# Kernel optimization log

Hardware: AMD Instinct MI355X
Metric: run time of the kernel (lower is better)

Reference implementation:

```python
import jax, jax.numpy as jnp
import numpy as np

N = 4096
INPUT_SIZE = 1024
HIDDEN = 512


def setup_inputs() -> dict:
    key = jax.random.key(0)
    ks = jax.random.split(key, 7)
    s_in = 1.0 / np.sqrt(INPUT_SIZE)
    return {
        "embs": jax.random.normal(ks[0], (N, INPUT_SIZE), dtype=jnp.float32),
        "Wq": jax.random.uniform(ks[1], (HIDDEN, INPUT_SIZE), jnp.float32, -s_in, s_in),
        "bq": jax.random.uniform(ks[2], (HIDDEN,), jnp.float32, -s_in, s_in),
        "Wk": jax.random.uniform(ks[3], (HIDDEN, INPUT_SIZE), jnp.float32, -s_in, s_in),
        "bk": jax.random.uniform(ks[4], (HIDDEN,), jnp.float32, -s_in, s_in),
        "Wv": jax.random.uniform(ks[5], (HIDDEN, INPUT_SIZE), jnp.float32, -s_in, s_in),
        "bv": jax.random.uniform(ks[6], (HIDDEN,), jnp.float32, -s_in, s_in),
    }


def reference(embs, Wq, bq, Wk, bk, Wv, bv):
    # Linear projections (nn.Linear: x @ W.T + b)
    q = embs @ Wq.T + bq   # [N, H]
    k = embs @ Wk.T + bk   # [N, H]
    v = embs @ Wv.T + bv   # [N, H]
    # Unscaled attention scores, softmax over keys (dim=1)
    scores = jax.nn.softmax(q @ k.T, axis=1)  # [N, N]
    # Per-query weighted sum over values == scores @ v
    return scores @ v  # [N, H]
```

## Files before the change

kernel.cpp:

```cpp
#include <hip/hip_runtime.h>
#include <stdint.h>

#define NT 4096
#define DI 1024
#define DH 512

typedef _Float16 f16;
typedef _Float16 half8 __attribute__((ext_vector_type(8)));
typedef short short8 __attribute__((ext_vector_type(8)));
typedef float f32x4 __attribute__((ext_vector_type(4)));
typedef short s16;

__device__ __forceinline__ s16 to_bf16(float f) {
  uint32_t u = __builtin_bit_cast(uint32_t, f);
  u += 0x7FFFu + ((u >> 16) & 1u);
  return (s16)(u >> 16);
}
__device__ __forceinline__ float from_bf16(s16 s) {
  uint32_t u = ((uint32_t)(uint16_t)s) << 16;
  return __builtin_bit_cast(float, u);
}

__device__ __forceinline__ void gload_lds16(const void* g, void* l) {
  void* gnc = const_cast<void*>(g);
  __builtin_amdgcn_global_load_lds(
      (__attribute__((address_space(1))) void*)gnc,
      (__attribute__((address_space(3))) void*)l,
      16, 0, 0);
}

__global__ __launch_bounds__(256)
void cvt_all(const float4* __restrict__ e,  const float4* __restrict__ wq,
             const float4* __restrict__ wk, const float4* __restrict__ wv,
             half8* __restrict__ de, half8* __restrict__ dq,
             half8* __restrict__ dk, half8* __restrict__ dv) {
  int b = blockIdx.x;
  const float4* src; half8* dst; int i;
  if (b < 2048)      { src = e;  dst = de; i = b * 256 + threadIdx.x; }
  else if (b < 2304) { src = wq; dst = dq; i = (b - 2048) * 256 + threadIdx.x; }
  else if (b < 2560) { src = wk; dst = dk; i = (b - 2304) * 256 + threadIdx.x; }
  else               { src = wv; dst = dv; i = (b - 2560) * 256 + threadIdx.x; }
  float4 a = src[2 * i], c = src[2 * i + 1];
  half8 h;
  h[0] = (f16)a.x; h[1] = (f16)a.y; h[2] = (f16)a.z; h[3] = (f16)a.w;
  h[4] = (f16)c.x; h[5] = (f16)c.y; h[6] = (f16)c.z; h[7] = (f16)c.w;
  dst[i] = h;
}

__global__ __launch_bounds__(256)
void scores_qk(const s16* __restrict__ q, const s16* __restrict__ k,
               s16* __restrict__ P, float* __restrict__ Dpart)
{
  __shared__ __align__(16) s16 At[2][256 * 32];
  __shared__ __align__(16) s16 Bt[2][128 * 32];
  const int tid  = threadIdx.x;
  const int lane = tid & 63;
  const int wave = tid >> 6;
  const int bn = blockIdx.x * 128;
  const int bm = blockIdx.y * 256;
  const int frow = lane & 15;
  const int kslc = (lane >> 4) * 8;

  f32x4 acc[4][8];
#pragma unroll
  for (int i = 0; i < 4; ++i)
#pragma unroll
    for (int j = 0; j < 8; ++j) acc[i][j] = (f32x4){0.f, 0.f, 0.f, 0.f};

  auto stage = [&](int buf, int kt) {
#pragma unroll
    for (int c = 0; c < 4; ++c) {
      int e8 = c * 256 + tid;
      gload_lds16(q + (size_t)(bm + (e8 >> 2)) * 512 + kt * 32 + (e8 & 3) * 8,
                  &At[buf][e8 * 8]);
    }
#pragma unroll
    for (int c = 0; c < 2; ++c) {
      int e8 = c * 256 + tid;
      gload_lds16(k + (size_t)(bn + (e8 >> 2)) * 512 + kt * 32 + (e8 & 3) * 8,
                  &Bt[buf][e8 * 8]);
    }
  };

  stage(0, 0);
  __syncthreads();

  for (int kt = 0; kt < 16; ++kt) {
    const int cur = kt & 1;
    if (kt < 15) stage(cur ^ 1, kt + 1);
    half8 af[4], bf[8];
#pragma unroll
    for (int mi = 0; mi < 4; ++mi)
      af[mi] = *(const half8*)&At[cur][(wave * 64 + mi * 16 + frow) * 32 + kslc];
#pragma unroll
    for (int ni = 0; ni < 8; ++ni)
      bf[ni] = *(const half8*)&Bt[cur][(ni * 16 + frow) * 32 + kslc];
#pragma unroll
    for (int mi = 0; mi < 4; ++mi)
#pragma unroll
      for (int ni = 0; ni < 8; ++ni)
        acc[mi][ni] = __builtin_amdgcn_mfma_f32_16x16x32_f16(af[mi], bf[ni], acc[mi][ni], 0, 0, 0);
    __syncthreads();
  }

  const int rbase = (lane >> 4) * 4;
#pragma unroll
  for (int mi = 0; mi < 4; ++mi) {
#pragma unroll
    for (int j = 0; j < 4; ++j) {
      int gr = bm + wave * 64 + mi * 16 + rbase + j;
      float s4 = 0.f;
#pragma unroll
      for (int ni = 0; ni < 8; ++ni) {
        int gc = bn + ni * 16 + frow;
        float p = __expf(fminf(acc[mi][ni][j] - 45.f, 80.f));
        s16 pb = to_bf16(p);
        P[(size_t)gr * NT + gc] = pb;
        s4 += from_bf16(pb);
      }
      s4 += __shfl_xor(s4, 1);
      s4 += __shfl_xor(s4, 2);
      s4 += __shfl_xor(s4, 4);
      s4 += __shfl_xor(s4, 8);
      if (frow == 0) Dpart[(size_t)blockIdx.x * NT + gr] = s4;
    }
  }
}

template<int MODE>
__global__ __launch_bounds__(256)
void gemm_bt(const s16* __restrict__ A, const s16* __restrict__ B0,
             s16* __restrict__ O16,
             s16* __restrict__ oq, s16* __restrict__ ok, s16* __restrict__ ovT,
             const float* __restrict__ bq, const float* __restrict__ bk,
             const float* __restrict__ bv,
             int M, int Nn, int K, int lda, int ldb, int ldc)
{
  __shared__ __align__(16) s16 At[2][128 * 32];
  __shared__ __align__(16) s16 Bt[2][128 * 32];

  const int tid  = threadIdx.x;
  const int lane = tid & 63;
  const int wave = tid >> 6;
  const int wr = wave >> 1, wc = wave & 1;

  int bxi = blockIdx.x, byi = blockIdx.y, kchunk = 0;
  if (MODE == 2) {
    int bid = blockIdx.x;
    kchunk = bid & 3;
    bxi = (bid >> 2) & 3;
    byi = bid >> 4;
  }
  const int bm = byi * 128;
  const int bn = bxi * 128;

  const s16* Bmat = B0;
  const float* bias = nullptr;
  if (MODE == 1) {
    int z = blockIdx.z;
    Bmat = B0 + (size_t)z * DH * DI;
    bias = (z == 0) ? bq : (z == 1) ? bk : bv;
  }
  if (MODE == 2) {
    int koff = kchunk * K;
    A    += koff;
    Bmat  = B0 + koff;
  }

  const int frow = lane & 15;
  const int kslc = (lane >> 4) * 8;

  f32x4 acc[4][4];
#pragma unroll
  for (int i = 0; i < 4; ++i)
#pragma unroll
    for (int j = 0; j < 4; ++j) acc[i][j] = (f32x4){0.f, 0.f, 0.f, 0.f};

  const int nk = K >> 5;

  auto stage = [&](int buf, int kt) {
#pragma unroll
    for (int cc = 0; cc < 2; ++cc) {
      int c  = wave * 2 + cc;
      int e8 = c * 64 + lane;
      int r  = e8 >> 2;
      int c8 = e8 & 3;
      gload_lds16(A    + (size_t)(bm + r) * lda + kt * 32 + c8 * 8, &At[buf][c * 512]);
      gload_lds16(Bmat + (size_t)(bn + r) * ldb + kt * 32 + c8 * 8, &Bt[buf][c * 512]);
    }
  };

  stage(0, 0);
  __syncthreads();

  for (int kt = 0; kt < nk; ++kt) {
    const int cur = kt & 1;
    if (kt + 1 < nk) stage(cur ^ 1, kt + 1);
    short8 af[4], bf[4];
#pragma unroll
    for (int mi = 0; mi < 4; ++mi)
      af[mi] = *(const short8*)&At[cur][(wr * 64 + mi * 16 + frow) * 32 + kslc];
#pragma unroll
    for (int ni = 0; ni < 4; ++ni)
      bf[ni] = *(const short8*)&Bt[cur][(wc * 64 + ni * 16 + frow) * 32 + kslc];
#pragma unroll
    for (int mi = 0; mi < 4; ++mi)
#pragma unroll
      for (int ni = 0; ni < 4; ++ni) {
        if (MODE == 2)
          acc[mi][ni] = __builtin_amdgcn_mfma_f32_16x16x32_bf16(af[mi], bf[ni], acc[mi][ni], 0, 0, 0);
        else
          acc[mi][ni] = __builtin_amdgcn_mfma_f32_16x16x32_f16(
              __builtin_bit_cast(half8, af[mi]), __builtin_bit_cast(half8, bf[ni]),
              acc[mi][ni], 0, 0, 0);
      }
    __syncthreads();
  }

  const int rbase = (lane >> 4) * 4;
#pragma unroll
  for (int mi = 0; mi < 4; ++mi) {
#pragma unroll
    for (int j = 0; j < 4; ++j) {
      int gr = bm + wr * 64 + mi * 16 + rbase + j;
#pragma unroll
      for (int ni = 0; ni < 4; ++ni) {
        int gc = bn + wc * 64 + ni * 16 + frow;
        float v = acc[mi][ni][j];
        if (MODE == 1) {
          v += bias[gc];
          int z = blockIdx.z;
          if (z == 0)      oq[(size_t)gr * ldc + gc] = __builtin_bit_cast(s16, (f16)v);
          else if (z == 1) ok[(size_t)gr * ldc + gc] = __builtin_bit_cast(s16, (f16)v);
          else             ovT[(size_t)gc * M + gr] = to_bf16(v);
        } else {
          O16[(size_t)kchunk * NT * DH + (size_t)gr * DH + gc] = to_bf16(v);
        }
      }
    }
  }
}

__global__ __launch_bounds__(256)
void combine_pv(const s16* __restrict__ Np, const float* __restrict__ Dp,
                float* __restrict__ out) {
  int gi = blockIdx.x * 256 + threadIdx.x;
  int r  = gi >> 6;
  int d8 = (gi & 63) * 8;
  float D = 0.f;
#pragma unroll
  for (int p = 0; p < 32; ++p) D += Dp[(size_t)p * NT + r];
  float a[8];
#pragma unroll
  for (int j = 0; j < 8; ++j) a[j] = 0.f;
#pragma unroll
  for (int c = 0; c < 4; ++c) {
    short8 h = *(const short8*)&Np[(size_t)c * NT * DH + (size_t)r * DH + d8];
#pragma unroll
    for (int j = 0; j < 8; ++j) a[j] += from_bf16(h[j]);
  }
  float inv = 1.f / D;
  float4* o4 = (float4*)&out[(size_t)r * DH + d8];
  o4[0] = (float4){a[0] * inv, a[1] * inv, a[2] * inv, a[3] * inv};
  o4[1] = (float4){a[4] * inv, a[5] * inv, a[6] * inv, a[7] * inv};
}

extern "C" void kernel_launch(void* const* d_in, const int* in_sizes, int n_in,
                              void* d_out, int out_size, void* d_ws, size_t ws_size,
                              hipStream_t stream) {
  const float* embs = (const float*)d_in[0];
  const float* Wq   = (const float*)d_in[1];
  const float* bq   = (const float*)d_in[2];
  const float* Wk   = (const float*)d_in[3];
  const float* bk   = (const float*)d_in[4];
  const float* Wv   = (const float*)d_in[5];
  const float* bv   = (const float*)d_in[6];
  float* out = (float*)d_out;

  char* ws = (char*)d_ws;
  s16*   P      = (s16*)(ws);
  s16*   embs16 = (s16*)(ws);
  s16*   W16    = (s16*)(ws + 8388608);
  s16*   Npart  = (s16*)(ws + 33554432);
  float* Dpart  = (float*)(ws + 50331648);
  s16*   q16    = (s16*)(ws + 51380224);
  s16*   k16    = (s16*)(ws + 55574528);
  s16*   vT16   = (s16*)(ws + 59768832);

  cvt_all<<<2816, 256, 0, stream>>>(
      (const float4*)embs, (const float4*)Wq, (const float4*)Wk, (const float4*)Wv,
      (half8*)embs16, (half8*)W16, (half8*)(W16 + 524288), (half8*)(W16 + 1048576));

  gemm_bt<1><<<dim3(4, 32, 3), 256, 0, stream>>>(
      embs16, W16, nullptr, q16, k16, vT16, bq, bk, bv,
      4096, 512, 1024, 1024, 1024, 512);

  scores_qk<<<dim3(32, 16), 256, 0, stream>>>(q16, k16, P, Dpart);

  gemm_bt<2><<<dim3(512, 1, 1), 256, 0, stream>>>(
      P, vT16, Npart, nullptr, nullptr, nullptr, nullptr, nullptr, nullptr,
      4096, 512, 1024, 4096, 4096, 512);

  combine_pv<<<1024, 256, 0, stream>>>(Npart, Dpart, out);
}
```

Baseline: 174.7 us.

## Restructure QK scores kernel: 8 waves, triple-buffered K=64 stages, swizzled LDS

The scores kernel now uses 512 threads arranged as a 4x2 wave grid, each wave computing a 64x64 sub-tile. It loads 64-wide K slices into a three-stage LDS ring with explicit vmcnt waits, XOR-swizzles the LDS layout to avoid bank conflicts, and raises wave priority around the MFMA block. The row-sum partials double to 64 per row, so combine_pv now sums 64 entries. The aim is to hide global load latency and cut LDS conflicts, at the cost of about 144KB of LDS per block, which limits each CU to one block.

After: 172.4 us. No clear change (-1.3%).

```diff
diff --git a/kernel.cpp b/kernel.cpp
--- a/kernel.cpp
+++ b/kernel.cpp
@@ -47,60 +47,83 @@
   dst[i] = h;
 }
 
-__global__ __launch_bounds__(256)
+__global__ __launch_bounds__(512, 1)
 void scores_qk(const s16* __restrict__ q, const s16* __restrict__ k,
                s16* __restrict__ P, float* __restrict__ Dpart)
 {
-  __shared__ __align__(16) s16 At[2][256 * 32];
-  __shared__ __align__(16) s16 Bt[2][128 * 32];
+  __shared__ __align__(16) s16 At[3][256 * 64];
+  __shared__ __align__(16) s16 Bt[3][128 * 64];
   const int tid  = threadIdx.x;
   const int lane = tid & 63;
-  const int wave = tid >> 6;
+  const int wid  = tid >> 6;
+  const int wr = wid >> 1, wc = wid & 1;
   const int bn = blockIdx.x * 128;
   const int bm = blockIdx.y * 256;
   const int frow = lane & 15;
-  const int kslc = (lane >> 4) * 8;
-
-  f32x4 acc[4][8];
+  const int g16  = lane >> 4;
+
+  f32x4 acc[4][4];
 #pragma unroll
   for (int i = 0; i < 4; ++i)
 #pragma unroll
-    for (int j = 0; j < 8; ++j) acc[i][j] = (f32x4){0.f, 0.f, 0.f, 0.f};
-
-  auto stage = [&](int buf, int kt) {
+    for (int j = 0; j < 4; ++j) acc[i][j] = (f32x4){0.f, 0.f, 0.f, 0.f};
+
+  auto stage = [&](int s, int kt) {
 #pragma unroll
     for (int c = 0; c < 4; ++c) {
-      int e8 = c * 256 + tid;
-      gload_lds16(q + (size_t)(bm + (e8 >> 2)) * 512 + kt * 32 + (e8 & 3) * 8,
-                  &At[buf][e8 * 8]);
+      int u = c * 512 + tid;
+      int r = u >> 3, jp = u & 7, j = jp ^ (r & 7);
+      gload_lds16(q + (size_t)(bm + r) * 512 + kt * 64 + j * 8, &At[s][(size_t)u * 8]);
     }
 #pragma unroll
     for (int c = 0; c < 2; ++c) {
-      int e8 = c * 256 + tid;
-      gload_lds16(k + (size_t)(bn + (e8 >> 2)) * 512 + kt * 32 + (e8 & 3) * 8,
-                  &Bt[buf][e8 * 8]);
+      int u = c * 512 + tid;
+      int r = u >> 3, jp = u & 7, j = jp ^ (r & 7);
+      gload_lds16(k + (size_t)(bn + r) * 512 + kt * 64 + j * 8, &Bt[s][(size_t)u * 8]);
     }
   };
 
   stage(0, 0);
-  __syncthreads();
-
-  for (int kt = 0; kt < 16; ++kt) {
-    const int cur = kt & 1;
-    if (kt < 15) stage(cur ^ 1, kt + 1);
-    half8 af[4], bf[8];
-#pragma unroll
-    for (int mi = 0; mi < 4; ++mi)
-      af[mi] = *(const half8*)&At[cur][(wave * 64 + mi * 16 + frow) * 32 + kslc];
-#pragma unroll
-    for (int ni = 0; ni < 8; ++ni)
-      bf[ni] = *(const half8*)&Bt[cur][(ni * 16 + frow) * 32 + kslc];
-#pragma unroll
-    for (int mi = 0; mi < 4; ++mi)
-#pragma unroll
-      for (int ni = 0; ni < 8; ++ni)
-        acc[mi][ni] = __builtin_amdgcn_mfma_f32_16x16x32_f16(af[mi], bf[ni], acc[mi][ni], 0, 0, 0);
-    __syncthreads();
+  stage(1, 1);
+  asm volatile("s_waitcnt vmcnt(6)" ::: "memory");
+  __builtin_amdgcn_sched_barrier(0);
+  __builtin_amdgcn_s_barrier();
+
+#pragma unroll
+  for (int t = 0; t < 8; ++t) {
+    const int s = t % 3;
+    if (t + 2 < 8) stage((t + 2) % 3, t + 2);
+    if (t < 6) { asm volatile("s_waitcnt vmcnt(6)" ::: "memory"); }
+    else       { asm volatile("s_waitcnt vmcnt(0)" ::: "memory"); }
+    __builtin_amdgcn_sched_barrier(0);
+
+    half8 af[2][4], bf[2][4];
+#pragma unroll
+    for (int kk = 0; kk < 2; ++kk) {
+#pragma unroll
+      for (int mi = 0; mi < 4; ++mi) {
+        int r = wr * 64 + mi * 16 + frow;
+        int jb = (kk * 4 + g16) ^ (r & 7);
+        af[kk][mi] = *(const half8*)&At[s][(size_t)(r * 8 + jb) * 8];
+      }
+#pragma unroll
+      for (int ni = 0; ni < 4; ++ni) {
+        int r = wc * 64 + ni * 16 + frow;
+        int jb = (kk * 4 + g16) ^ (r & 7);
+        bf[kk][ni] = *(const half8*)&Bt[s][(size_t)(r * 8 + jb) * 8];
+      }
+    }
+    __builtin_amdgcn_s_setprio(1);
+#pragma unroll
+    for (int kk = 0; kk < 2; ++kk)
+#pragma unroll
+      for (int mi = 0; mi < 4; ++mi)
+#pragma unroll
+        for (int ni = 0; ni < 4; ++ni)
+          acc[mi][ni] = __builtin_amdgcn_mfma_f32_16x16x32_f16(
+              af[kk][mi], bf[kk][ni], acc[mi][ni], 0, 0, 0);
+    __builtin_amdgcn_s_setprio(0);
+    __builtin_amdgcn_s_barrier();
   }
 
   const int rbase = (lane >> 4) * 4;
@@ -108,11 +131,11 @@
   for (int mi = 0; mi < 4; ++mi) {
 #pragma unroll
     for (int j = 0; j < 4; ++j) {
-      int gr = bm + wave * 64 + mi * 16 + rbase + j;
+      int gr = bm + wr * 64 + mi * 16 + rbase + j;
       float s4 = 0.f;
 #pragma unroll
-      for (int ni = 0; ni < 8; ++ni) {
-        int gc = bn + ni * 16 + frow;
+      for (int ni = 0; ni < 4; ++ni) {
+        int gc = bn + wc * 64 + ni * 16 + frow;
         float p = __expf(fminf(acc[mi][ni][j] - 45.f, 80.f));
         s16 pb = to_bf16(p);
         P[(size_t)gr * NT + gc] = pb;
@@ -122,7 +145,7 @@
       s4 += __shfl_xor(s4, 2);
       s4 += __shfl_xor(s4, 4);
       s4 += __shfl_xor(s4, 8);
-      if (frow == 0) Dpart[(size_t)blockIdx.x * NT + gr] = s4;
+      if (frow == 0) Dpart[(size_t)(blockIdx.x * 2 + wc) * NT + gr] = s4;
     }
   }
 }
@@ -249,7 +272,7 @@
   int d8 = (gi & 63) * 8;
   float D = 0.f;
 #pragma unroll
-  for (int p = 0; p < 32; ++p) D += Dp[(size_t)p * NT + r];
+  for (int p = 0; p < 64; ++p) D += Dp[(size_t)p * NT + r];
   float a[8];
 #pragma unroll
   for (int j = 0; j < 8; ++j) a[j] = 0.f;
@@ -295,7 +318,7 @@
       embs16, W16, nullptr, q16, k16, vT16, bq, bk, bv,
       4096, 512, 1024, 1024, 1024, 512);
 
-  scores_qk<<<dim3(32, 16), 256, 0, stream>>>(q16, k16, P, Dpart);
+  scores_qk<<<dim3(32, 16), 512, 0, stream>>>(q16, k16, P, Dpart);
 
   gemm_bt<2><<<dim3(512, 1, 1), 256, 0, stream>>>(
       P, vT16, Npart, nullptr, nullptr, nullptr, nullptr, nullptr, nullptr,
```
